# Performance work log

Measured on AMD Instinct MI355X. Metric: run time of the kernel, lower is better.

## Reference

```python
import jax, jax.numpy as jnp
import numpy as np

EMBED = 1024
HEADS = 16
HEAD_DIM = EMBED // HEADS


def setup_inputs() -> dict:
    key = jax.random.key(0)
    ks = jax.random.split(key, 7)
    B, S = 4, 2048
    q = jax.random.normal(ks[0], (B, S, EMBED), dtype=jnp.float32)
    k = jax.random.normal(ks[1], (B, S, EMBED), dtype=jnp.float32)
    v = jax.random.normal(ks[2], (B, S, EMBED), dtype=jnp.float32)
    # causal mask, broadcast over heads: [B, 1, S, S]
    mask = jnp.broadcast_to(jnp.tril(jnp.ones((S, S), dtype=jnp.int32))[None, None], (B, 1, S, S))
    scale = 1.0 / np.sqrt(EMBED)
    w_q = jax.random.normal(ks[3], (EMBED, EMBED), dtype=jnp.float32) * scale
    w_k = jax.random.normal(ks[4], (EMBED, EMBED), dtype=jnp.float32) * scale
    w_v = jax.random.normal(ks[5], (EMBED, EMBED), dtype=jnp.float32) * scale
    w_o = jax.random.normal(ks[6], (EMBED, EMBED), dtype=jnp.float32) * scale
    return {"q": q, "k": k, "v": v, "mask": mask,
            "w_q": w_q, "w_k": w_k, "w_v": w_v, "w_o": w_o}


def reference(q, k, v, mask, w_q, w_k, w_v, w_o):
    B, S, _ = q.shape
    # Linear projections (torch Linear: x @ W^T), split into heads: [B,H,S,D]
    def proj(x, w):
        return (x @ w.T).reshape(B, -1, HEADS, HEAD_DIM).transpose(0, 2, 1, 3)
    qh, kh, vh = proj(q, w_q), proj(k, w_k), proj(v, w_v)
    scores = jnp.einsum('bhqd,bhkd->bhqk', qh, kh) / jnp.sqrt(jnp.float32(HEAD_DIM))
    scores = jnp.where(mask == 0, jnp.float32(-1e9), scores)
    attn = jax.nn.softmax(scores, axis=-1)
    # dropout is identity in eval/reference mode
    x = jnp.einsum('bhqk,bhkd->bhqd', attn, vh)  # [B,H,S,D]
    x = x.transpose(0, 2, 1, 3).reshape(B, S, HEADS * HEAD_DIM)
    return x @ w_o.T
```

## Files before the change

kernel.cpp:

```cpp
#include <hip/hip_runtime.h>

typedef unsigned short u16;
typedef __attribute__((ext_vector_type(8))) short v8s;
typedef __attribute__((ext_vector_type(4))) float v4f;

#define S_LEN  2048
#define NHEADS 16
#define DHEAD  64
#define EMB    1024

#if __has_builtin(__builtin_amdgcn_exp2f)
#define EXP2F __builtin_amdgcn_exp2f
#else
#define EXP2F exp2f
#endif

__device__ __forceinline__ u16 f32_bf16(float f) {
  union { float f; unsigned u; } x; x.f = f;
  unsigned r = x.u + 0x7fffu + ((x.u >> 16) & 1u);
  return (u16)(r >> 16);
}

__device__ __forceinline__ void async16(const void* g, void* l) {
  __builtin_amdgcn_global_load_lds(
      (const __attribute__((address_space(1))) unsigned int*)g,
      (__attribute__((address_space(3))) unsigned int*)l, 16, 0, 0);
}

__global__ __launch_bounds__(256) void cvt_all(
    const float4* __restrict__ s0, const float4* __restrict__ s1,
    const float4* __restrict__ s2, const float4* __restrict__ s3,
    const float4* __restrict__ s4, const float4* __restrict__ s5,
    const float4* __restrict__ s6,
    ushort4* __restrict__ d0, ushort4* __restrict__ d1,
    ushort4* __restrict__ d2, ushort4* __restrict__ d3,
    ushort4* __restrict__ d4, ushort4* __restrict__ d5,
    ushort4* __restrict__ d6, int nbig, int nsmall) {
  const int y = blockIdx.y;
  const float4* s; ushort4* d;
  switch (y) {
    case 0: s = s0; d = d0; break;  case 1: s = s1; d = d1; break;
    case 2: s = s2; d = d2; break;  case 3: s = s3; d = d3; break;
    case 4: s = s4; d = d4; break;  case 5: s = s5; d = d5; break;
    default: s = s6; d = d6; break;
  }
  const int n4 = (y < 3) ? nbig : nsmall;
  for (int i = blockIdx.x * 256 + threadIdx.x; i < n4; i += gridDim.x * 256) {
    const float4 v = s[i];
    ushort4 o;
    o.x = f32_bf16(v.x); o.y = f32_bf16(v.y);
    o.z = f32_bf16(v.z); o.w = f32_bf16(v.w);
    d[i] = o;
  }
}

template <int MODE>
__global__ __launch_bounds__(256, 2) void gemm2ph(
    const u16* __restrict__ A, const u16* __restrict__ W0,
    const u16* __restrict__ W1, const u16* __restrict__ W2,
    u16* __restrict__ Cq, u16* __restrict__ Ck, u16* __restrict__ Cv,
    float* __restrict__ Cf, int mtiles) {
  const int K = 1024;
  const int NKT = 16;
  __shared__ __align__(16) u16 lA[2][128 * 64];
  __shared__ __align__(16) u16 lB[2][128 * 64];
  const int t = threadIdx.x;
  const int lane = t & 63, wv = t >> 6;
  const int wm = wv >> 1, wn = wv & 1;
  const int qr = lane >> 4, cl = lane & 15;

  const int nwg = gridDim.x;
  const int sid = (blockIdx.x & 7) * (nwg >> 3) + (blockIdx.x >> 3);
  const int bm = sid % mtiles, bn = sid / mtiles;
  const int m0 = bm << 7, n0 = bn << 7;
  const int sec = (MODE == 0) ? (m0 >> 13) : 0;
  const u16* W =
      (MODE == 0) ? ((sec == 0) ? W0 : (sec == 1) ? W1 : W2) : W0;

  v4f acc[4][4];
#pragma unroll
  for (int i = 0; i < 4; ++i)
#pragma unroll
    for (int j = 0; j < 4; ++j) acc[i][j] = (v4f){0.f, 0.f, 0.f, 0.f};

  const int srow = t >> 3;
  const int sw = ((t & 7) ^ (srow & 7)) << 3;
  const u16* aS[4];
  const u16* bS[4];
#pragma unroll
  for (int u = 0; u < 4; ++u) {
    aS[u] = A + (size_t)(m0 + srow + u * 32) * K + sw;
    bS[u] = W + (size_t)(n0 + srow + u * 32) * K + sw;
  }

#pragma unroll
  for (int u = 0; u < 4; ++u) async16(aS[u], &lA[0][(t + (u << 8)) << 3]);
#pragma unroll
  for (int u = 0; u < 4; ++u) async16(bS[u], &lB[0][(t + (u << 8)) << 3]);
  __syncthreads();

  for (int kt = 0; kt < NKT; ++kt) {
    const int cur = kt & 1;
    if (kt + 1 < NKT) {
      const int off = (kt + 1) << 6;
#pragma unroll
      for (int u = 0; u < 4; ++u)
        async16(aS[u] + off, &lA[1 - cur][(t + (u << 8)) << 3]);
#pragma unroll
      for (int u = 0; u < 4; ++u)
        async16(bS[u] + off, &lB[1 - cur][(t + (u << 8)) << 3]);
    }
    v8s a[4][2], b[4][2];
#pragma unroll
    for (int mf = 0; mf < 4; ++mf)
#pragma unroll
      for (int kh = 0; kh < 2; ++kh) {
        const int R = wm * 64 + mf * 16 + cl;
        a[mf][kh] =
            *(const v8s*)&lA[cur][R * 64 + ((((kh << 2) + qr) ^ (R & 7)) << 3)];
      }
#pragma unroll
    for (int nf = 0; nf < 4; ++nf)
#pragma unroll
      for (int kh = 0; kh < 2; ++kh) {
        const int R = wn * 64 + nf * 16 + cl;
        b[nf][kh] =
            *(const v8s*)&lB[cur][R * 64 + ((((kh << 2) + qr) ^ (R & 7)) << 3)];
      }
    __builtin_amdgcn_s_setprio(1);
#pragma unroll
    for (int kh = 0; kh < 2; ++kh)
#pragma unroll
      for (int mf = 0; mf < 4; ++mf)
#pragma unroll
        for (int nf = 0; nf < 4; ++nf)
          acc[mf][nf] = __builtin_amdgcn_mfma_f32_16x16x32_bf16(
              a[mf][kh], b[nf][kh], acc[mf][nf], 0, 0, 0);
    __builtin_amdgcn_s_setprio(0);
    __syncthreads();
  }

  if constexpr (MODE == 0) {
    u16* C = (sec == 0) ? Cq : (sec == 1) ? Ck : Cv;
#pragma unroll
    for (int mf = 0; mf < 4; ++mf)
#pragma unroll
      for (int nf = 0; nf < 4; ++nf)
#pragma unroll
        for (int r = 0; r < 4; ++r) {
          const int mloc = (m0 & 8191) + wm * 64 + mf * 16 + qr * 4 + r;
          const int n = n0 + wn * 64 + nf * 16 + cl;
          const int bb = mloc >> 11, s = mloc & (S_LEN - 1);
          const int h = n >> 6, d = n & (DHEAD - 1);
          const size_t idx =
              (sec < 2) ? (((size_t)bb * NHEADS + h) * S_LEN + s) * DHEAD + d
                        : (((size_t)bb * NHEADS + h) * DHEAD + d) * S_LEN + s;
          C[idx] = f32_bf16(acc[mf][nf][r]);
        }
  } else {
#pragma unroll
    for (int mf = 0; mf < 4; ++mf)
#pragma unroll
      for (int nf = 0; nf < 4; ++nf)
#pragma unroll
        for (int r = 0; r < 4; ++r) {
          const int m = m0 + wm * 64 + mf * 16 + qr * 4 + r;
          const int n = n0 + wn * 64 + nf * 16 + cl;
          Cf[(size_t)m * 1024 + n] = acc[mf][nf][r];
        }
  }
}

__global__ __launch_bounds__(256) void attn_causal(const u16* __restrict__ Qp,
                                                   const u16* __restrict__ Kp,
                                                   const u16* __restrict__ VpT,
                                                   u16* __restrict__ Out) {
  __shared__ __align__(16) u16 lK[2][64 * 64];
  __shared__ __align__(16) u16 lV[2][64 * 64];
  __shared__ __align__(16) u16 pb[4][32 * 64];
  const int t = threadIdx.x;
  const int lane = t & 63, w = t >> 6;
  const int qr = lane >> 4, cl = lane & 15;
  const int id = blockIdx.x;
  const int col = (id & 7) + ((id >> 6) << 3);
  const int pair = (id >> 3) & 7;
  const int h = col & 15, b = col >> 4;
  const size_t bh = ((size_t)b * NHEADS + h) * S_LEN * DHEAD;
  const u16* Qb = Qp + bh;
  const u16* Kb = Kp + bh;
  const u16* Vb = VpT + bh;

  v8s vone;
#pragma unroll
  for (int j = 0; j < 8; ++j) vone[j] = (short)0x3F80;
  const float SC = 0.125f * 1.4426950408889634f;

  for (int phase = 0; phase < 2; ++phase) {
    const int qt = phase == 0 ? (15 - pair) : pair;
    const int q0 = qt << 7;
    const int wr0 = q0 + w * 32;

    v8s aq[2][2];
#pragma unroll
    for (int mf = 0; mf < 2; ++mf)
#pragma unroll
      for (int kf = 0; kf < 2; ++kf)
        aq[mf][kf] = *(const v8s*)(Qb + (size_t)(wr0 + mf * 16 + cl) * DHEAD +
                                   kf * 32 + qr * 8);

    v4f o[2][4], lac[2];
#pragma unroll
    for (int mf = 0; mf < 2; ++mf) {
      lac[mf] = (v4f){0.f, 0.f, 0.f, 0.f};
#pragma unroll
      for (int nf = 0; nf < 4; ++nf) o[mf][nf] = (v4f){0.f, 0.f, 0.f, 0.f};
    }

    const int nkt = 2 * qt + 2;
    __syncthreads();
#pragma unroll
    for (int i = 0; i < 2; ++i) {
      const int c = t + (i << 8);
      const int krow = c >> 3, kdc = (c & 7) ^ (krow & 7);
      async16(Kb + (size_t)krow * DHEAD + kdc * 8, &lK[0][(w * 64 + (i << 8)) * 8]);
      const int vd = c >> 3, vkc = (c & 7) ^ (vd & 7);
      async16(Vb + (size_t)vd * S_LEN + vkc * 8, &lV[0][(w * 64 + (i << 8)) * 8]);
    }

    for (int kt = 0; kt < nkt; ++kt) {
      const int k0 = kt << 6;
      const int cb = kt & 1;
      __syncthreads();
      if (kt + 1 < nkt) {
        const int kn = (kt + 1) << 6;
#pragma unroll
        for (int i = 0; i < 2; ++i) {
          const int c = t + (i << 8);
          const int krow = c >> 3, kdc = (c & 7) ^ (krow & 7);
          async16(Kb + (size_t)(kn + krow) * DHEAD + kdc * 8,
                  &lK[1 - cb][(w * 64 + (i << 8)) * 8]);
          const int vd = c >> 3, vkc = (c & 7) ^ (vd & 7);
          async16(Vb + (size_t)vd * S_LEN + kn + vkc * 8,
                  &lV[1 - cb][(w * 64 + (i << 8)) * 8]);
        }
      }
      if (k0 > wr0 + 31) continue;

      v4f sacc[2][4];
#pragma unroll
      for (int mf = 0; mf < 2; ++mf)
#pragma unroll
        for (int ni = 0; ni < 4; ++ni) sacc[mf][ni] = (v4f){0.f, 0.f, 0.f, 0.f};
#pragma unroll
      for (int kf = 0; kf < 2; ++kf)
#pragma unroll
        for (int ni = 0; ni < 4; ++ni) {
          const v8s bk = *(const v8s*)&lK[cb][((ni * 16 + cl) * 8 +
                                              (((kf << 2) + qr) ^ (cl & 7))) * 8];
          sacc[0][ni] = __builtin_amdgcn_mfma_f32_16x16x32_bf16(aq[0][kf], bk,
                                                                sacc[0][ni], 0, 0, 0);
          sacc[1][ni] = __builtin_amdgcn_mfma_f32_16x16x32_bf16(aq[1][kf], bk,
                                                                sacc[1][ni], 0, 0, 0);
        }

#pragma unroll
      for (int mf = 0; mf < 2; ++mf) {
        const int rowb0 = wr0 + mf * 16;
        if (k0 + 63 <= rowb0) {
#pragma unroll
          for (int ni = 0; ni < 4; ++ni) {
            const int kc = ni * 2 + (cl >> 3);
#pragma unroll
            for (int r = 0; r < 4; ++r) {
              const float e = EXP2F(sacc[mf][ni][r] * SC);
              pb[w][((kc * 32 + mf * 16 + r * 4 + qr) << 3) + (cl & 7)] =
                  (u16)(__float_as_uint(e) >> 16);
            }
          }
        } else {
          const int rowb = rowb0 + qr * 4;
#pragma unroll
          for (int ni = 0; ni < 4; ++ni) {
            const int colk = k0 + ni * 16 + cl;
            const int kc = ni * 2 + (cl >> 3);
#pragma unroll
            for (int r = 0; r < 4; ++r) {
              float e = EXP2F(sacc[mf][ni][r] * SC);
              if (colk > rowb + r) e = 0.f;
              pb[w][((kc * 32 + mf * 16 + r * 4 + qr) << 3) + (cl & 7)] =
                  (u16)(__float_as_uint(e) >> 16);
            }
          }
        }
      }

#pragma unroll
      for (int kf = 0; kf < 2; ++kf) {
        const int kc = (kf << 2) + qr;
        const int sig0 = ((cl & 3) << 2) + (cl >> 2);
        const v8s ap0 = *(const v8s*)&pb[w][((kc * 32 + sig0) << 3)];
        const v8s ap1 = *(const v8s*)&pb[w][((kc * 32 + 16 + sig0) << 3)];
        lac[0] = __builtin_amdgcn_mfma_f32_16x16x32_bf16(ap0, vone, lac[0], 0, 0, 0);
        lac[1] = __builtin_amdgcn_mfma_f32_16x16x32_bf16(ap1, vone, lac[1], 0, 0, 0);
#pragma unroll
        for (int nf = 0; nf < 4; ++nf) {
          const v8s bv = *(const v8s*)&lV[cb][((nf * 16 + cl) * 8 +
                                              (kc ^ (cl & 7))) * 8];
          o[0][nf] = __builtin_amdgcn_mfma_f32_16x16x32_bf16(ap0, bv, o[0][nf], 0, 0, 0);
          o[1][nf] = __builtin_amdgcn_mfma_f32_16x16x32_bf16(ap1, bv, o[1][nf], 0, 0, 0);
        }
      }
    }

#pragma unroll
    for (int mf = 0; mf < 2; ++mf) {
      float inv[4];
#pragma unroll
      for (int r = 0; r < 4; ++r) inv[r] = 1.0f / lac[mf][r];
#pragma unroll
      for (int nf = 0; nf < 4; ++nf)
#pragma unroll
        for (int r = 0; r < 4; ++r) {
          const int row = wr0 + mf * 16 + qr * 4 + r;
          const int colo = h * DHEAD + nf * 16 + cl;
          Out[((size_t)b * S_LEN + row) * EMB + colo] = f32_bf16(o[mf][nf][r] * inv[r]);
        }
    }
  }
}

extern "C" void kernel_launch(void* const* d_in, const int* in_sizes, int n_in,
                              void* d_out, int out_size, void* d_ws, size_t ws_size,
                              hipStream_t stream) {
  (void)in_sizes; (void)n_in; (void)out_size; (void)ws_size;
  const float* q  = (const float*)d_in[0];
  const float* k  = (const float*)d_in[1];
  const float* v  = (const float*)d_in[2];
  const float* wq = (const float*)d_in[4];
  const float* wk = (const float*)d_in[5];
  const float* wv = (const float*)d_in[6];
  const float* wo = (const float*)d_in[7];
  float* out = (float*)d_out;

  const size_t MT = (size_t)4 * S_LEN * EMB;
  const size_t WT = (size_t)EMB * EMB;
  u16* p = (u16*)d_ws;
  u16* xq = p; p += MT;
  u16* xk = p; p += MT;
  u16* xv = p; p += MT;
  u16* wqb = p; p += WT;
  u16* wkb = p; p += WT;
  u16* wvb = p; p += WT;
  u16* wob = p; p += WT;
  u16* Qp = p; p += MT;
  u16* Kp = p; p += MT;
  u16* Vp = p; p += MT;
  u16* Ao = xq;

  const dim3 blk(256);
  hipLaunchKernelGGL(cvt_all, dim3(512, 7), blk, 0, stream,
                     (const float4*)q, (const float4*)k, (const float4*)v,
                     (const float4*)wq, (const float4*)wk, (const float4*)wv,
                     (const float4*)wo,
                     (ushort4*)xq, (ushort4*)xk, (ushort4*)xv,
                     (ushort4*)wqb, (ushort4*)wkb, (ushort4*)wvb, (ushort4*)wob,
                     (int)(MT / 4), (int)(WT / 4));
  hipLaunchKernelGGL((gemm2ph<0>), dim3(1536), blk, 0, stream,
                     xq, wqb, wkb, wvb, Qp, Kp, Vp, (float*)nullptr, 192);
  hipLaunchKernelGGL(attn_causal, dim3(512), blk, 0, stream, Qp, Kp, Vp, Ao);
  hipLaunchKernelGGL((gemm2ph<1>), dim3(512), blk, 0, stream,
                     Ao, wob, (const u16*)nullptr, (const u16*)nullptr,
                     (u16*)nullptr, (u16*)nullptr, (u16*)nullptr, out, 64);
}
```

Baseline: 348.0 us.

## Use triple-buffered K32 GEMM pipeline with explicit vmcnt waits and XCD tile mapping

The projection GEMMs move from a double-buffered K=64 tile loop with a full __syncthreads per step to a three-stage LDS ring of K=32 tiles. Loads are issued two tiles ahead and waited on with explicit s_waitcnt vmcnt plus a raw barrier. Smaller LDS use allows launch bounds of 3 blocks per CU, and the block-to-tile mapping is reworked so each XCD owns contiguous M tiles across all 8 N tiles. The aim is more memory/compute overlap and higher occupancy, at the cost of twice as many barriers per K and a hand-managed wait count that must match the number of outstanding loads.

```diff
diff --git a/kernel.cpp b/kernel.cpp
--- a/kernel.cpp
+++ b/kernel.cpp
@@ -26,6 +26,8 @@
       (const __attribute__((address_space(1))) unsigned int*)g,
       (__attribute__((address_space(3))) unsigned int*)l, 16, 0, 0);
 }
+
+#define FENCE() asm volatile("" ::: "memory")
 
 __global__ __launch_bounds__(256) void cvt_all(
     const float4* __restrict__ s0, const float4* __restrict__ s1,
@@ -55,24 +57,23 @@
 }
 
 template <int MODE>
-__global__ __launch_bounds__(256, 2) void gemm2ph(
+__global__ __launch_bounds__(256, 3) void gemm3b(
     const u16* __restrict__ A, const u16* __restrict__ W0,
     const u16* __restrict__ W1, const u16* __restrict__ W2,
     u16* __restrict__ Cq, u16* __restrict__ Ck, u16* __restrict__ Cv,
     float* __restrict__ Cf, int mtiles) {
   const int K = 1024;
-  const int NKT = 16;
-  __shared__ __align__(16) u16 lA[2][128 * 64];
-  __shared__ __align__(16) u16 lB[2][128 * 64];
+  const int NKT = 32;
+  __shared__ __align__(16) u16 lA[3][4096];
+  __shared__ __align__(16) u16 lB[3][4096];
   const int t = threadIdx.x;
   const int lane = t & 63, wv = t >> 6;
   const int wm = wv >> 1, wn = wv & 1;
   const int qr = lane >> 4, cl = lane & 15;
 
-  const int nwg = gridDim.x;
-  const int sid = (blockIdx.x & 7) * (nwg >> 3) + (blockIdx.x >> 3);
-  const int bm = sid % mtiles, bn = sid / mtiles;
-  const int m0 = bm << 7, n0 = bn << 7;
+  const int xcd = blockIdx.x & 7, q = blockIdx.x >> 3;
+  const int mt = xcd * (mtiles >> 3) + (q >> 3), nt = q & 7;
+  const int m0 = mt << 7, n0 = nt << 7;
   const int sec = (MODE == 0) ? (m0 >> 13) : 0;
   const u16* W =
       (MODE == 0) ? ((sec == 0) ? W0 : (sec == 1) ? W1 : W2) : W0;
@@ -83,62 +84,78 @@
 #pragma unroll
     for (int j = 0; j < 4; ++j) acc[i][j] = (v4f){0.f, 0.f, 0.f, 0.f};
 
-  const int srow = t >> 3;
-  const int sw = ((t & 7) ^ (srow & 7)) << 3;
-  const u16* aS[4];
-  const u16* bS[4];
-#pragma unroll
-  for (int u = 0; u < 4; ++u) {
-    aS[u] = A + (size_t)(m0 + srow + u * 32) * K + sw;
-    bS[u] = W + (size_t)(n0 + srow + u * 32) * K + sw;
-  }
-
-#pragma unroll
-  for (int u = 0; u < 4; ++u) async16(aS[u], &lA[0][(t + (u << 8)) << 3]);
-#pragma unroll
-  for (int u = 0; u < 4; ++u) async16(bS[u], &lB[0][(t + (u << 8)) << 3]);
-  __syncthreads();
-
-  for (int kt = 0; kt < NKT; ++kt) {
-    const int cur = kt & 1;
-    if (kt + 1 < NKT) {
-      const int off = (kt + 1) << 6;
-#pragma unroll
-      for (int u = 0; u < 4; ++u)
-        async16(aS[u] + off, &lA[1 - cur][(t + (u << 8)) << 3]);
-#pragma unroll
-      for (int u = 0; u < 4; ++u)
-        async16(bS[u] + off, &lB[1 - cur][(t + (u << 8)) << 3]);
-    }
-    v8s a[4][2], b[4][2];
-#pragma unroll
-    for (int mf = 0; mf < 4; ++mf)
-#pragma unroll
-      for (int kh = 0; kh < 2; ++kh) {
-        const int R = wm * 64 + mf * 16 + cl;
-        a[mf][kh] =
-            *(const v8s*)&lA[cur][R * 64 + ((((kh << 2) + qr) ^ (R & 7)) << 3)];
-      }
-#pragma unroll
-    for (int nf = 0; nf < 4; ++nf)
-#pragma unroll
-      for (int kh = 0; kh < 2; ++kh) {
-        const int R = wn * 64 + nf * 16 + cl;
-        b[nf][kh] =
-            *(const v8s*)&lB[cur][R * 64 + ((((kh << 2) + qr) ^ (R & 7)) << 3)];
-      }
-    __builtin_amdgcn_s_setprio(1);
-#pragma unroll
-    for (int kh = 0; kh < 2; ++kh)
-#pragma unroll
-      for (int mf = 0; mf < 4; ++mf)
-#pragma unroll
-        for (int nf = 0; nf < 4; ++nf)
-          acc[mf][nf] = __builtin_amdgcn_mfma_f32_16x16x32_bf16(
-              a[mf][kh], b[nf][kh], acc[mf][nf], 0, 0, 0);
-    __builtin_amdgcn_s_setprio(0);
-    __syncthreads();
-  }
+  const int Lt = t >> 3;
+  const int pt = (t & 7) ^ (Lt & 7);
+  const int rh = (pt >> 2) << 6;
+  const int kc8 = (pt & 3) << 3;
+  const u16* aS[2];
+  const u16* bS[2];
+#pragma unroll
+  for (int u = 0; u < 2; ++u) {
+    aS[u] = A + (size_t)(m0 + Lt + u * 32 + rh) * K + kc8;
+    bS[u] = W + (size_t)(n0 + Lt + u * 32 + rh) * K + kc8;
+  }
+  u16* const lA0 = &lA[0][0];
+  u16* const lB0 = &lB[0][0];
+
+  int aOff[4], bOff[4];
+#pragma unroll
+  for (int f = 0; f < 4; ++f) {
+    aOff[f] = (f * 16 + cl) * 64 + ((((wm << 2) | qr) ^ (cl & 7)) << 3);
+    bOff[f] = (f * 16 + cl) * 64 + ((((wn << 2) | qr) ^ (cl & 7)) << 3);
+  }
+
+#define STAGE3(TILE, BUF)                                                     \
+  do {                                                                        \
+    const int ka_ = (TILE) << 5;                                              \
+    u16* da_ = lA0 + (BUF) * 4096;                                            \
+    u16* db_ = lB0 + (BUF) * 4096;                                            \
+    async16(aS[0] + ka_, da_ + t * 8);                                        \
+    async16(aS[1] + ka_, da_ + (t + 256) * 8);                                \
+    async16(bS[0] + ka_, db_ + t * 8);                                        \
+    async16(bS[1] + ka_, db_ + (t + 256) * 8);                                \
+  } while (0)
+
+#define BODY3(CUR)                                                            \
+  do {                                                                        \
+    const u16* ra_ = lA0 + (CUR) * 4096;                                      \
+    const u16* rb_ = lB0 + (CUR) * 4096;                                      \
+    v8s a_[4], b_[4];                                                         \
+    _Pragma("unroll") for (int mf = 0; mf < 4; ++mf)                          \
+        a_[mf] = *(const v8s*)(ra_ + aOff[mf]);                               \
+    _Pragma("unroll") for (int nf = 0; nf < 4; ++nf)                          \
+        b_[nf] = *(const v8s*)(rb_ + bOff[nf]);                               \
+    __builtin_amdgcn_s_setprio(1);                                            \
+    _Pragma("unroll") for (int mf = 0; mf < 4; ++mf)                          \
+        _Pragma("unroll") for (int nf = 0; nf < 4; ++nf)                      \
+            acc[mf][nf] = __builtin_amdgcn_mfma_f32_16x16x32_bf16(            \
+                a_[mf], b_[nf], acc[mf][nf], 0, 0, 0);                        \
+    __builtin_amdgcn_s_setprio(0);                                            \
+  } while (0)
+
+  STAGE3(0, 0);
+  STAGE3(1, 1);
+  FENCE();
+
+  int cur = 0, stg = 2;
+  for (int kt = 0; kt < NKT - 1; ++kt) {
+    asm volatile("s_waitcnt vmcnt(4)" ::: "memory");
+    FENCE();
+    __builtin_amdgcn_s_barrier();
+    FENCE();
+    if (kt < NKT - 2) STAGE3(kt + 2, stg);
+    BODY3(cur);
+    cur = (cur == 2) ? 0 : cur + 1;
+    stg = (stg == 2) ? 0 : stg + 1;
+  }
+  asm volatile("s_waitcnt vmcnt(0)" ::: "memory");
+  FENCE();
+  __builtin_amdgcn_s_barrier();
+  FENCE();
+  BODY3(cur);
+
+#undef STAGE3
+#undef BODY3
 
   if constexpr (MODE == 0) {
     u16* C = (sec == 0) ? Cq : (sec == 1) ? Ck : Cv;
@@ -365,10 +382,10 @@
                      (ushort4*)xq, (ushort4*)xk, (ushort4*)xv,
                      (ushort4*)wqb, (ushort4*)wkb, (ushort4*)wvb, (ushort4*)wob,
                      (int)(MT / 4), (int)(WT / 4));
-  hipLaunchKernelGGL((gemm2ph<0>), dim3(1536), blk, 0, stream,
+  hipLaunchKernelGGL((gemm3b<0>), dim3(1536), blk, 0, stream,
                      xq, wqb, wkb, wvb, Qp, Kp, Vp, (float*)nullptr, 192);
   hipLaunchKernelGGL(attn_causal, dim3(512), blk, 0, stream, Qp, Kp, Vp, Ao);
-  hipLaunchKernelGGL((gemm2ph<1>), dim3(512), blk, 0, stream,
+  hipLaunchKernelGGL((gemm3b<1>), dim3(512), blk, 0, stream,
                      Ao, wob, (const u16*)nullptr, (const u16*)nullptr,
                      (u16*)nullptr, (u16*)nullptr, (u16*)nullptr, out, 64);
 }
```

Result: slower. 362.8 us (+4.3%).

## Stage two KV tiles per barrier in attention and remap GEMM tile order per XCD

Applied to the files above, without the earlier changes.

The attention loop now loads and processes two 64-key tiles per synchronization group, with double-buffered groups. This halves the number of barriers and deepens the prefetch, at the cost of twice the LDS for K/V, and the kernel now asks for 2 blocks per CU. The GEMM tile mapping changes so each XCD takes a contiguous range of M tiles and walks 8 N tiles, aiming at better L2 reuse of A rows. The new mapping assumes the N dimension has exactly 8 tiles and that the grid matches mtiles*8.

```diff
diff --git a/kernel.cpp b/kernel.cpp
--- a/kernel.cpp
+++ b/kernel.cpp
@@ -69,10 +69,9 @@
   const int wm = wv >> 1, wn = wv & 1;
   const int qr = lane >> 4, cl = lane & 15;
 
-  const int nwg = gridDim.x;
-  const int sid = (blockIdx.x & 7) * (nwg >> 3) + (blockIdx.x >> 3);
-  const int bm = sid % mtiles, bn = sid / mtiles;
-  const int m0 = bm << 7, n0 = bn << 7;
+  const int xcd = blockIdx.x & 7, q = blockIdx.x >> 3;
+  const int mt = xcd * (mtiles >> 3) + (q >> 3), nt = q & 7;
+  const int m0 = mt << 7, n0 = nt << 7;
   const int sec = (MODE == 0) ? (m0 >> 13) : 0;
   const u16* W =
       (MODE == 0) ? ((sec == 0) ? W0 : (sec == 1) ? W1 : W2) : W0;
@@ -171,12 +170,11 @@
   }
 }
 
-__global__ __launch_bounds__(256) void attn_causal(const u16* __restrict__ Qp,
-                                                   const u16* __restrict__ Kp,
-                                                   const u16* __restrict__ VpT,
-                                                   u16* __restrict__ Out) {
-  __shared__ __align__(16) u16 lK[2][64 * 64];
-  __shared__ __align__(16) u16 lV[2][64 * 64];
+__global__ __launch_bounds__(256, 2) void attn_causal(
+    const u16* __restrict__ Qp, const u16* __restrict__ Kp,
+    const u16* __restrict__ VpT, u16* __restrict__ Out) {
+  __shared__ __align__(16) u16 lK[2][2][64 * 64];
+  __shared__ __align__(16) u16 lV[2][2][64 * 64];
   __shared__ __align__(16) u16 pb[4][32 * 64];
   const int t = threadIdx.x;
   const int lane = t & 63, w = t >> 6;
@@ -195,6 +193,20 @@
   for (int j = 0; j < 8; ++j) vone[j] = (short)0x3F80;
   const float SC = 0.125f * 1.4426950408889634f;
 
+#define STAGE_T(TILE, GP, SL)                                                 \
+  do {                                                                        \
+    const int kn_ = (TILE) << 6;                                              \
+    _Pragma("unroll") for (int i_ = 0; i_ < 2; ++i_) {                        \
+      const int c_ = t + (i_ << 8);                                           \
+      const int krow_ = c_ >> 3, kdc_ = (c_ & 7) ^ (krow_ & 7);               \
+      async16(Kb + (size_t)(kn_ + krow_) * DHEAD + kdc_ * 8,                  \
+              &lK[GP][SL][(w * 64 + (i_ << 8)) * 8]);                         \
+      const int vd_ = c_ >> 3, vkc_ = (c_ & 7) ^ (vd_ & 7);                   \
+      async16(Vb + (size_t)vd_ * S_LEN + kn_ + vkc_ * 8,                      \
+              &lV[GP][SL][(w * 64 + (i_ << 8)) * 8]);                         \
+    }                                                                         \
+  } while (0)
+
   for (int phase = 0; phase < 2; ++phase) {
     const int qt = phase == 0 ? (15 - pair) : pair;
     const int q0 = qt << 7;
@@ -216,98 +228,89 @@
       for (int nf = 0; nf < 4; ++nf) o[mf][nf] = (v4f){0.f, 0.f, 0.f, 0.f};
     }
 
-    const int nkt = 2 * qt + 2;
+    const int ngrp = qt + 1;
     __syncthreads();
-#pragma unroll
-    for (int i = 0; i < 2; ++i) {
-      const int c = t + (i << 8);
-      const int krow = c >> 3, kdc = (c & 7) ^ (krow & 7);
-      async16(Kb + (size_t)krow * DHEAD + kdc * 8, &lK[0][(w * 64 + (i << 8)) * 8]);
-      const int vd = c >> 3, vkc = (c & 7) ^ (vd & 7);
-      async16(Vb + (size_t)vd * S_LEN + vkc * 8, &lV[0][(w * 64 + (i << 8)) * 8]);
-    }
-
-    for (int kt = 0; kt < nkt; ++kt) {
-      const int k0 = kt << 6;
-      const int cb = kt & 1;
+    STAGE_T(0, 0, 0);
+    STAGE_T(1, 0, 1);
+
+    for (int g = 0; g < ngrp; ++g) {
+      const int gp = g & 1;
       __syncthreads();
-      if (kt + 1 < nkt) {
-        const int kn = (kt + 1) << 6;
-#pragma unroll
-        for (int i = 0; i < 2; ++i) {
-          const int c = t + (i << 8);
-          const int krow = c >> 3, kdc = (c & 7) ^ (krow & 7);
-          async16(Kb + (size_t)(kn + krow) * DHEAD + kdc * 8,
-                  &lK[1 - cb][(w * 64 + (i << 8)) * 8]);
-          const int vd = c >> 3, vkc = (c & 7) ^ (vd & 7);
-          async16(Vb + (size_t)vd * S_LEN + kn + vkc * 8,
-                  &lV[1 - cb][(w * 64 + (i << 8)) * 8]);
-        }
+      if (g + 1 < ngrp) {
+        STAGE_T(2 * g + 2, 1 - gp, 0);
+        STAGE_T(2 * g + 3, 1 - gp, 1);
       }
-      if (k0 > wr0 + 31) continue;
-
-      v4f sacc[2][4];
-#pragma unroll
-      for (int mf = 0; mf < 2; ++mf)
-#pragma unroll
-        for (int ni = 0; ni < 4; ++ni) sacc[mf][ni] = (v4f){0.f, 0.f, 0.f, 0.f};
-#pragma unroll
-      for (int kf = 0; kf < 2; ++kf)
-#pragma unroll
-        for (int ni = 0; ni < 4; ++ni) {
-          const v8s bk = *(const v8s*)&lK[cb][((ni * 16 + cl) * 8 +
-                                              (((kf << 2) + qr) ^ (cl & 7))) * 8];
-          sacc[0][ni] = __builtin_amdgcn_mfma_f32_16x16x32_bf16(aq[0][kf], bk,
-                                                                sacc[0][ni], 0, 0, 0);
-          sacc[1][ni] = __builtin_amdgcn_mfma_f32_16x16x32_bf16(aq[1][kf], bk,
-                                                                sacc[1][ni], 0, 0, 0);
-        }
-
-#pragma unroll
-      for (int mf = 0; mf < 2; ++mf) {
-        const int rowb0 = wr0 + mf * 16;
-        if (k0 + 63 <= rowb0) {
+#pragma unroll
+      for (int sl = 0; sl < 2; ++sl) {
+        const int kt = 2 * g + sl;
+        const int k0 = kt << 6;
+        if (k0 > wr0 + 31) continue;
+        const u16* lKc = &lK[gp][sl][0];
+        const u16* lVc = &lV[gp][sl][0];
+
+        v4f sacc[2][4];
+#pragma unroll
+        for (int mf = 0; mf < 2; ++mf)
+#pragma unroll
+          for (int ni = 0; ni < 4; ++ni) sacc[mf][ni] = (v4f){0.f, 0.f, 0.f, 0.f};
+#pragma unroll
+        for (int kf = 0; kf < 2; ++kf)
 #pragma unroll
           for (int ni = 0; ni < 4; ++ni) {
-            const int kc = ni * 2 + (cl >> 3);
-#pragma unroll
-            for (int r = 0; r < 4; ++r) {
-              const float e = EXP2F(sacc[mf][ni][r] * SC);
-              pb[w][((kc * 32 + mf * 16 + r * 4 + qr) << 3) + (cl & 7)] =
-                  (u16)(__float_as_uint(e) >> 16);
+            const v8s bk = *(const v8s*)&lKc[((ni * 16 + cl) * 8 +
+                                             (((kf << 2) + qr) ^ (cl & 7))) * 8];
+            sacc[0][ni] = __builtin_amdgcn_mfma_f32_16x16x32_bf16(
+                aq[0][kf], bk, sacc[0][ni], 0, 0, 0);
+            sacc[1][ni] = __builtin_amdgcn_mfma_f32_16x16x32_bf16(
+                aq[1][kf], bk, sacc[1][ni], 0, 0, 0);
+          }
+
+#pragma unroll
+        for (int mf = 0; mf < 2; ++mf) {
+          const int rowb0 = wr0 + mf * 16;
+          if (k0 + 63 <= rowb0) {
+#pragma unroll
+            for (int ni = 0; ni < 4; ++ni) {
+              const int kc = ni * 2 + (cl >> 3);
+#pragma unroll
+              for (int r = 0; r < 4; ++r) {
+                const float e = EXP2F(sacc[mf][ni][r] * SC);
+                pb[w][((kc * 32 + mf * 16 + r * 4 + qr) << 3) + (cl & 7)] =
+                    (u16)(__float_as_uint(e) >> 16);
+              }
+            }
+          } else {
+            const int rowb = rowb0 + qr * 4;
+#pragma unroll
+            for (int ni = 0; ni < 4; ++ni) {
+              const int colk = k0 + ni * 16 + cl;
+              const int kc = ni * 2 + (cl >> 3);
+#pragma unroll
+              for (int r = 0; r < 4; ++r) {
+                float e = EXP2F(sacc[mf][ni][r] * SC);
+                if (colk > rowb + r) e = 0.f;
+                pb[w][((kc * 32 + mf * 16 + r * 4 + qr) << 3) + (cl & 7)] =
+                    (u16)(__float_as_uint(e) >> 16);
+              }
             }
           }
-        } else {
-          const int rowb = rowb0 + qr * 4;
-#pragma unroll
-          for (int ni = 0; ni < 4; ++ni) {
-            const int colk = k0 + ni * 16 + cl;
-            const int kc = ni * 2 + (cl >> 3);
-#pragma unroll
-            for (int r = 0; r < 4; ++r) {
-              float e = EXP2F(sacc[mf][ni][r] * SC);
-              if (colk > rowb + r) e = 0.f;
-              pb[w][((kc * 32 + mf * 16 + r * 4 + qr) << 3) + (cl & 7)] =
-                  (u16)(__float_as_uint(e) >> 16);
-            }
+        }
+
+#pragma unroll
+        for (int kf = 0; kf < 2; ++kf) {
+          const int kc = (kf << 2) + qr;
+          const int sig0 = ((cl & 3) << 2) + (cl >> 2);
+          const v8s ap0 = *(const v8s*)&pb[w][((kc * 32 + sig0) << 3)];
+          const v8s ap1 = *(const v8s*)&pb[w][((kc * 32 + 16 + sig0) << 3)];
+          lac[0] = __builtin_amdgcn_mfma_f32_16x16x32_bf16(ap0, vone, lac[0], 0, 0, 0);
+          lac[1] = __builtin_amdgcn_mfma_f32_16x16x32_bf16(ap1, vone, lac[1], 0, 0, 0);
+#pragma unroll
+          for (int nf = 0; nf < 4; ++nf) {
+            const v8s bv = *(const v8s*)&lVc[((nf * 16 + cl) * 8 +
+                                             (kc ^ (cl & 7))) * 8];
+            o[0][nf] = __builtin_amdgcn_mfma_f32_16x16x32_bf16(ap0, bv, o[0][nf], 0, 0, 0);
+            o[1][nf] = __builtin_amdgcn_mfma_f32_16x16x32_bf16(ap1, bv, o[1][nf], 0, 0, 0);
           }
-        }
-      }
-
-#pragma unroll
-      for (int kf = 0; kf < 2; ++kf) {
-        const int kc = (kf << 2) + qr;
-        const int sig0 = ((cl & 3) << 2) + (cl >> 2);
-        const v8s ap0 = *(const v8s*)&pb[w][((kc * 32 + sig0) << 3)];
-        const v8s ap1 = *(const v8s*)&pb[w][((kc * 32 + 16 + sig0) << 3)];
-        lac[0] = __builtin_amdgcn_mfma_f32_16x16x32_bf16(ap0, vone, lac[0], 0, 0, 0);
-        lac[1] = __builtin_amdgcn_mfma_f32_16x16x32_bf16(ap1, vone, lac[1], 0, 0, 0);
-#pragma unroll
-        for (int nf = 0; nf < 4; ++nf) {
-          const v8s bv = *(const v8s*)&lV[cb][((nf * 16 + cl) * 8 +
-                                              (kc ^ (cl & 7))) * 8];
-          o[0][nf] = __builtin_amdgcn_mfma_f32_16x16x32_bf16(ap0, bv, o[0][nf], 0, 0, 0);
-          o[1][nf] = __builtin_amdgcn_mfma_f32_16x16x32_bf16(ap1, bv, o[1][nf], 0, 0, 0);
         }
       }
     }
@@ -327,6 +330,7 @@
         }
     }
   }
+#undef STAGE_T
 }
 
 extern "C" void kernel_launch(void* const* d_in, const int* in_sizes, int n_in,
```

New measurement: 349.5 us. About the same (+0.4%).
